# Kernel optimization log

Measured on AMD Instinct MI355X. Metric: run time of the kernel, lower is better.

## Reference

```python
import jax, jax.numpy as jnp
import numpy as np

C = 256
NUM_HEADS = 8
GROUPS = 32
EPS = 1e-5


def setup_inputs() -> dict:
    key = jax.random.key(0)
    ks = jax.random.split(key, 7)
    B, D, H, W = 1, 16, 16, 16
    x = jax.random.normal(ks[0], (B, C, D, H, W), dtype=jnp.float32)
    # GroupNorm affine params (torch default: weight=1, bias=0; randomize slightly)
    gn_gamma = 1.0 + 0.02 * jax.random.normal(ks[1], (C,), dtype=jnp.float32)
    gn_beta = 0.02 * jax.random.normal(ks[2], (C,), dtype=jnp.float32)
    # 1x1x1 Conv3d == pointwise linear over channels
    qkv_w = jax.random.normal(ks[3], (3 * C, C), dtype=jnp.float32) / np.sqrt(C)
    qkv_b = 0.01 * jax.random.normal(ks[4], (3 * C,), dtype=jnp.float32)
    proj_w = jax.random.normal(ks[5], (C, C), dtype=jnp.float32) / np.sqrt(C)
    proj_b = 0.01 * jax.random.normal(ks[6], (C,), dtype=jnp.float32)
    return {"x": x, "gn_gamma": gn_gamma, "gn_beta": gn_beta,
            "qkv_w": qkv_w, "qkv_b": qkv_b, "proj_w": proj_w, "proj_b": proj_b}


def _group_norm(x, gamma, beta):
    B, Cc, D, H, W = x.shape
    xg = x.reshape(B, GROUPS, -1)  # [B, G, (C/G)*D*H*W]
    mean = xg.mean(axis=2, keepdims=True)
    var = xg.var(axis=2, keepdims=True)
    xn = ((xg - mean) * jax.lax.rsqrt(var + EPS)).reshape(B, Cc, D, H, W)
    return xn * gamma[None, :, None, None, None] + beta[None, :, None, None, None]


def reference(x, gn_gamma, gn_beta, qkv_w, qkv_b, proj_w, proj_b):
    B, Cc, D, H, W = x.shape
    N = D * H * W
    heads = NUM_HEADS
    hd = Cc // heads
    scale = hd ** -0.5

    xn = _group_norm(x, gn_gamma, gn_beta)
    # 1x1x1 conv -> pointwise linear over channel dim
    h = jnp.einsum('bcn,oc->bon', xn.reshape(B, Cc, N), qkv_w) + qkv_b[None, :, None]
    # match torch: reshape(B,3,heads,hd,N).permute(1,0,2,4,3)
    qkv = h.reshape(B, 3, heads, hd, N).transpose(1, 0, 2, 4, 3)  # [3,B,heads,N,hd]
    q, k, v = qkv[0], qkv[1], qkv[2]
    attn = jax.nn.softmax(jnp.einsum('bhnd,bhmd->bhnm', q, k) * scale, axis=-1)
    out = jnp.einsum('bhnm,bhmd->bhnd', attn, v)  # [B,heads,N,hd]
    # match torch: transpose(1,2).reshape(B,C,D,H,W)
    out = out.transpose(0, 2, 1, 3).reshape(B, Cc, D, H, W)
    out = jnp.einsum('bcn,oc->bon', out.reshape(B, Cc, N), proj_w) + proj_b[None, :, None]
    return x + out.reshape(B, Cc, D, H, W)
```

## Files before the change

kernel.cpp:

```cpp
#include <hip/hip_runtime.h>
#include <hip/hip_bf16.h>
#include <cstddef>
#include <cstdint>

#define NTOK 4096
#define CCH  256
#define HEADS 8
#define HD    32
#define QSCALE 0.25503494f

typedef __attribute__((ext_vector_type(8)))  short short8;
typedef __attribute__((ext_vector_type(4)))  short short4v;
typedef __attribute__((ext_vector_type(16))) float f32x16;

__device__ __forceinline__ unsigned short f2bf(float x) {
    unsigned u = __builtin_bit_cast(unsigned, x);
    u = (u + 0x7fffu + ((u >> 16) & 1u)) >> 16;
    return (unsigned short)u;
}
__device__ __forceinline__ unsigned packbf2(float a, float b) {
    unsigned r;
    asm("v_cvt_pk_bf16_f32 %0, %1, %2" : "=v"(r) : "v"(a), "v"(b));
    return r;
}
__device__ __forceinline__ float exp2hw(float x) {
    float r;
    asm("v_exp_f32 %0, %1" : "=v"(r) : "v"(x));
    return r;
}

#define GLDS(gsrc, ldst) \
  __builtin_amdgcn_global_load_lds((const __attribute__((address_space(1))) unsigned int*)(const void*)(gsrc), \
                                   (__attribute__((address_space(3))) unsigned int*)(void*)(ldst), 16, 0, 0)

#define CROW(r, hi) (((r) & 3) + 8 * ((r) >> 2) + 4 * (hi))

__global__ __launch_bounds__(256) void gn_part_kernel(
    const float* __restrict__ X, float2* __restrict__ part)
{
    int c = blockIdx.x, tid = threadIdx.x;
    const float4* xr = (const float4*)(X + (size_t)c * NTOK);
    float s = 0.f, ss = 0.f;
    #pragma unroll
    for (int i = 0; i < 4; i++) {
        float4 v = xr[tid + i * 256];
        s  += (v.x + v.y) + (v.z + v.w);
        ss += (v.x*v.x + v.y*v.y) + (v.z*v.z + v.w*v.w);
    }
    #pragma unroll
    for (int off = 32; off >= 1; off >>= 1) {
        s  += __shfl_down(s, off, 64);
        ss += __shfl_down(ss, off, 64);
    }
    __shared__ float rs[4], rss[4];
    int wid = tid >> 6, lane = tid & 63;
    if (lane == 0) { rs[wid] = s; rss[wid] = ss; }
    __syncthreads();
    if (tid == 0) {
        part[c] = make_float2(rs[0] + rs[1] + rs[2] + rs[3],
                              rss[0] + rss[1] + rss[2] + rss[3]);
    }
}

__global__ __launch_bounds__(256) void prep_kernel(
    const float* __restrict__ X, const float2* __restrict__ part,
    const float* __restrict__ gamma, const float* __restrict__ beta,
    const float* __restrict__ qkvw, const float* __restrict__ projw,
    unsigned short* __restrict__ Xt, unsigned short* __restrict__ Wqb,
    unsigned short* __restrict__ Wpb)
{
    int bi = blockIdx.x, tid = threadIdx.x;
    if (bi >= 256) {
        const float* src; unsigned short* dst;
        if (bi < 268) { src = qkvw + (size_t)(bi - 256) * 16384; dst = Wqb + (size_t)(bi - 256) * 16384; }
        else          { src = projw + (size_t)(bi - 268) * 16384; dst = Wpb + (size_t)(bi - 268) * 16384; }
        #pragma unroll
        for (int i = 0; i < 16; i++) {
            float4 v = *(const float4*)(src + (size_t)tid * 4 + (size_t)i * 1024);
            short4v w;
            w[0] = (short)f2bf(v.x); w[1] = (short)f2bf(v.y);
            w[2] = (short)f2bf(v.z); w[3] = (short)f2bf(v.w);
            *(short4v*)(dst + (size_t)tid * 4 + (size_t)i * 1024) = w;
        }
        return;
    }
    __shared__ float plds[64 * 65];
    __shared__ float gmean[8], grstd[8];
    int ci = bi >> 6, ni = bi & 63;
    if (tid < 8) {
        int g = ci * 8 + tid;
        float s = 0.f, ss = 0.f;
        #pragma unroll
        for (int k = 0; k < 8; k++) {
            float2 p = part[g * 8 + k];
            s += p.x; ss += p.y;
        }
        float mean = s * (1.f / 32768.f);
        float var  = ss * (1.f / 32768.f) - mean * mean;
        gmean[tid] = mean;
        grstd[tid] = rsqrtf(var + 1e-5f);
    }
    __syncthreads();
    #pragma unroll
    for (int i = 0; i < 4; i++) {
        int cl = (tid >> 4) + i * 16;
        int c  = ci * 64 + cl;
        int gl = cl >> 3;
        float scv = gamma[c] * grstd[gl];
        float tcv = beta[c] - gmean[gl] * scv;
        float4 v = *(const float4*)(X + (size_t)c * NTOK + ni * 64 + (tid & 15) * 4);
        float* row = plds + cl * 65 + (tid & 15) * 4;
        row[0] = v.x * scv + tcv; row[1] = v.y * scv + tcv;
        row[2] = v.z * scv + tcv; row[3] = v.w * scv + tcv;
    }
    __syncthreads();
    int nw = tid >> 2, c4 = (tid & 3) * 16;
    unsigned short tmp[16];
    #pragma unroll
    for (int i = 0; i < 16; i++) tmp[i] = f2bf(plds[(c4 + i) * 65 + nw]);
    unsigned short* dst = Xt + (size_t)(ni * 64 + nw) * CCH + ci * 64 + c4;
    *(short8*)dst       = *(short8*)&tmp[0];
    *(short8*)(dst + 8) = *(short8*)&tmp[8];
}

__global__ __launch_bounds__(256) void qkv_mfma_kernel(
    const unsigned short* __restrict__ Wqb, const unsigned short* __restrict__ Xt,
    const float* __restrict__ qkvb,
    unsigned short* __restrict__ Qb, unsigned short* __restrict__ Kbf,
    unsigned short* __restrict__ Vtb)
{
    __shared__ __align__(16) char vlds[16384];
    const int tid = threadIdx.x;
    const int wid = tid >> 6, lane = tid & 63;
    const int l31 = lane & 31, hi = lane >> 5;
    const int bo = blockIdx.x >> 5, ng = blockIdx.x & 31;
    const int o0 = bo * 32;
    const int n0 = ng * 128 + wid * 32;

    const unsigned short* ap = Xt + (size_t)(n0 + l31) * CCH + hi * 8;
    const unsigned short* bp = Wqb + (size_t)(o0 + l31) * CCH + hi * 8;

    f32x16 acc;
    #pragma unroll
    for (int i = 0; i < 16; i++) acc[i] = 0.f;
    #pragma unroll 4
    for (int ks = 0; ks < 16; ks++) {
        short8 af = *(const short8*)(ap + ks * 16);
        short8 bf = *(const short8*)(bp + ks * 16);
        acc = __builtin_amdgcn_mfma_f32_32x32x16_bf16(af, bf, acc, 0, 0, 0);
    }

    const int t3 = bo >> 3;
    const int h  = (o0 >> 5) & 7;
    const float bias = qkvb[o0 + l31];

    if (t3 != 2) {
        unsigned short* dst = ((t3 == 0) ? Qb : Kbf) + (size_t)h * NTOK * HD + l31;
        const float scl = (t3 == 0) ? QSCALE : 1.0f;
        #pragma unroll
        for (int r = 0; r < 16; r++) {
            int n = n0 + CROW(r, hi);
            dst[(size_t)n * HD] = f2bf((acc[r] + bias) * scl);
        }
    } else {
        char* my = vlds + wid * 4096;
        #pragma unroll
        for (int r = 0; r < 16; r++) {
            int row = CROW(r, hi);
            *(float*)(my + row * 128 + ((l31 * 4) ^ ((row & 7) << 4))) = acc[r] + bias;
        }
        unsigned short tmp[16];
        #pragma unroll
        for (int i = 0; i < 16; i++) {
            int n = hi * 16 + i;
            tmp[i] = f2bf(*(const float*)(my + n * 128 + ((l31 * 4) ^ ((n & 7) << 4))));
        }
        unsigned short* vd = Vtb + ((size_t)h * HD + l31) * NTOK + n0 + hi * 16;
        *(short8*)vd       = *(short8*)&tmp[0];
        *(short8*)(vd + 8) = *(short8*)&tmp[8];
    }
}

__global__ __launch_bounds__(256, 2) void attn_mfma_kernel(
    const unsigned short* __restrict__ Qb, const unsigned short* __restrict__ Kbf,
    const unsigned short* __restrict__ Vtb, unsigned short* __restrict__ att_t)
{
    __shared__ __align__(16) char ldsbuf[65536];
    __shared__ float lsum[4][64];
    const int tid = threadIdx.x;
    const int wid = tid >> 6, lane = tid & 63;
    const int l31 = lane & 31, hi = lane >> 5;
    const int bid = blockIdx.x;
    const int h    = bid & 7;
    const int g    = bid >> 3;
    const int base = g & 15;
    const int j0   = (g >> 4) * 64;

    const char* Khb = (const char*)(Kbf + (size_t)h * NTOK * HD) + (size_t)wid * 65536;
    const char* Vhb = (const char*)(Vtb + (size_t)h * HD * NTOK) + (size_t)wid * 2048;

    const char* srcK0 = Khb + l31 * 64 + hi * 16;
    const char* srcK1 = Khb + l31 * 64 + 32 + hi * 16;
    const char* srcV0 = Vhb + (size_t)l31 * 8192 + hi * 16;
    const char* srcV1 = Vhb + (size_t)l31 * 8192 + 32 + hi * 16;
    char* myLDS = ldsbuf + wid * 16384;

#define STAGE(tt, bb) do { \
    char* _db = myLDS + (bb) * 4096; \
    GLDS(srcK0 + (size_t)(tt) * 2048, _db); \
    GLDS(srcK1 + (size_t)(tt) * 2048, _db + 1024); \
    GLDS(srcV0 + (size_t)(tt) * 64,   _db + 2048); \
    GLDS(srcV1 + (size_t)(tt) * 64,   _db + 3072); \
} while (0)

    const int koff0 = l31 * 16 + hi * 512;
    const int koff1 = l31 * 16 + 1024 + hi * 512;
    const int voff0 = 2048 + koff0;
    const int voff1 = 2048 + koff1;

    const unsigned short* qpA = Qb + ((size_t)h * NTOK + base + 16 * (size_t)(j0 + l31)) * HD + hi * 8;
    const unsigned short* qpB = qpA + (size_t)32 * 16 * HD;
    short8 qfA0 = *(const short8*)qpA;
    short8 qfA1 = *(const short8*)(qpA + 16);
    short8 qfB0 = *(const short8*)qpB;
    short8 qfB1 = *(const short8*)(qpB + 16);

    f32x16 oaccA, oaccB;
    #pragma unroll
    for (int i = 0; i < 16; i++) { oaccA[i] = 0.f; oaccB[i] = 0.f; }
    const f32x16 zero = oaccA;
    float lA = 0.f, lB = 0.f;

    STAGE(0, 0);
    STAGE(1, 1);
    STAGE(2, 2);

    #pragma unroll 1
    for (int t = 0; t < 32; t++) {
        asm volatile("s_waitcnt vmcnt(8)" ::: "memory");
        const int ts = (t + 3 < 32) ? (t + 3) : 31;
        STAGE(ts, (t + 3) & 3);

        const char* kb = myLDS + (t & 3) * 4096;
        short8 kf0 = *(const short8*)(kb + koff0);
        short8 kf1 = *(const short8*)(kb + koff1);

        f32x16 sA = __builtin_amdgcn_mfma_f32_32x32x16_bf16(kf0, qfA0, zero, 0, 0, 0);
        f32x16 sB = __builtin_amdgcn_mfma_f32_32x32x16_bf16(kf0, qfB0, zero, 0, 0, 0);
        sA = __builtin_amdgcn_mfma_f32_32x32x16_bf16(kf1, qfA1, sA, 0, 0, 0);
        sB = __builtin_amdgcn_mfma_f32_32x32x16_bf16(kf1, qfB1, sB, 0, 0, 0);

        short8 vf0 = *(const short8*)(kb + voff0);
        short8 vf1 = *(const short8*)(kb + voff1);

        float pA[16], pB[16];
        #pragma unroll
        for (int r = 0; r < 16; r++) pA[r] = exp2hw(sA[r]);
        #pragma unroll
        for (int r = 0; r < 16; r++) pB[r] = exp2hw(sB[r]);
        lA += (((pA[0]+pA[1]) + (pA[2]+pA[3])) + ((pA[4]+pA[5]) + (pA[6]+pA[7])))
            + (((pA[8]+pA[9]) + (pA[10]+pA[11])) + ((pA[12]+pA[13]) + (pA[14]+pA[15])));
        lB += (((pB[0]+pB[1]) + (pB[2]+pB[3])) + ((pB[4]+pB[5]) + (pB[6]+pB[7])))
            + (((pB[8]+pB[9]) + (pB[10]+pB[11])) + ((pB[12]+pB[13]) + (pB[14]+pB[15])));

        #pragma unroll
        for (int m = 0; m < 2; m++) {
            const int b8 = m * 8;
            unsigned A0 = packbf2(pA[b8 + 0], pA[b8 + 1]);
            unsigned A1 = packbf2(pA[b8 + 2], pA[b8 + 3]);
            unsigned B0 = packbf2(pA[b8 + 4], pA[b8 + 5]);
            unsigned B1 = packbf2(pA[b8 + 6], pA[b8 + 7]);
            asm volatile("v_permlane32_swap_b32 %0, %1" : "+v"(A0), "+v"(B0));
            asm volatile("v_permlane32_swap_b32 %0, %1" : "+v"(A1), "+v"(B1));
            union { unsigned u[4]; short8 v; } pa;
            pa.u[0] = A0; pa.u[1] = A1; pa.u[2] = B0; pa.u[3] = B1;
            oaccA = __builtin_amdgcn_mfma_f32_32x32x16_bf16(
                pa.v, (m == 0) ? vf0 : vf1, oaccA, 0, 0, 0);
        }
        #pragma unroll
        for (int m = 0; m < 2; m++) {
            const int b8 = m * 8;
            unsigned A0 = packbf2(pB[b8 + 0], pB[b8 + 1]);
            unsigned A1 = packbf2(pB[b8 + 2], pB[b8 + 3]);
            unsigned B0 = packbf2(pB[b8 + 4], pB[b8 + 5]);
            unsigned B1 = packbf2(pB[b8 + 6], pB[b8 + 7]);
            asm volatile("v_permlane32_swap_b32 %0, %1" : "+v"(A0), "+v"(B0));
            asm volatile("v_permlane32_swap_b32 %0, %1" : "+v"(A1), "+v"(B1));
            union { unsigned u[4]; short8 v; } pa;
            pa.u[0] = A0; pa.u[1] = A1; pa.u[2] = B0; pa.u[3] = B1;
            oaccB = __builtin_amdgcn_mfma_f32_32x32x16_bf16(
                pa.v, (m == 0) ? vf0 : vf1, oaccB, 0, 0, 0);
        }
    }
#undef STAGE

    lA += __shfl_xor(lA, 32, 64);
    lB += __shfl_xor(lB, 32, 64);
    char* st = myLDS;
    #pragma unroll
    for (int r = 0; r < 16; r++) {
        int rowA = CROW(r, hi);
        *(float*)(st + rowA * 148 + l31 * 4) = oaccA[r];
        *(float*)(st + (rowA + 32) * 148 + l31 * 4) = oaccB[r];
    }
    if (lane < 32) { lsum[wid][l31] = lA; lsum[wid][32 + l31] = lB; }
    __syncthreads();

    const int d = tid >> 3, q8 = (tid & 7) * 8;
    unsigned short ob[8];
    #pragma unroll
    for (int i = 0; i < 8; i++) {
        int q = q8 + i;
        float lt = (lsum[0][q] + lsum[1][q]) + (lsum[2][q] + lsum[3][q]);
        int so = q * 148 + d * 4;
        float a = (*(const float*)(ldsbuf + so)          + *(const float*)(ldsbuf + 16384 + so))
                + (*(const float*)(ldsbuf + 32768 + so)  + *(const float*)(ldsbuf + 49152 + so));
        ob[i] = f2bf(a / lt);
    }
    unsigned short* dst = att_t + (size_t)(base * 256 + h * 32 + d) * CCH + j0 + q8;
    *(short8*)dst = *(short8*)ob;
}

__global__ __launch_bounds__(256) void proj_mfma_kernel(
    const unsigned short* __restrict__ Wpb, const unsigned short* __restrict__ att_t,
    const float* __restrict__ X, const float* __restrict__ pb,
    float* __restrict__ out)
{
    const int tid = threadIdx.x;
    const int wid = tid >> 6, lane = tid & 63;
    const int l31 = lane & 31, hi = lane >> 5;
    const int ot = blockIdx.x >> 5, pg = blockIdx.x & 31;
    const int o0 = ot * 32;
    const int p0 = pg * 128 + wid * 32;

    const unsigned short* ap = Wpb + (size_t)(o0 + l31) * CCH + hi * 8;
    const unsigned short* bp = att_t + (size_t)(p0 + l31) * CCH + hi * 8;

    f32x16 acc;
    #pragma unroll
    for (int i = 0; i < 16; i++) acc[i] = 0.f;
    #pragma unroll 4
    for (int ks = 0; ks < 16; ks++) {
        short8 af = *(const short8*)(ap + ks * 16);
        short8 bf = *(const short8*)(bp + ks * 16);
        acc = __builtin_amdgcn_mfma_f32_32x32x16_bf16(af, bf, acc, 0, 0, 0);
    }
    #pragma unroll
    for (int r = 0; r < 16; r++) {
        int o = o0 + CROW(r, hi);
        size_t ofs = (size_t)o * NTOK + p0 + l31;
        out[ofs] = X[ofs] + pb[o] + acc[r];
    }
}

extern "C" void kernel_launch(void* const* d_in, const int* in_sizes, int n_in,
                              void* d_out, int out_size, void* d_ws, size_t ws_size,
                              hipStream_t stream)
{
    const float* x     = (const float*)d_in[0];
    const float* gamma = (const float*)d_in[1];
    const float* beta  = (const float*)d_in[2];
    const float* qkvw  = (const float*)d_in[3];
    const float* qkvb  = (const float*)d_in[4];
    const float* projw = (const float*)d_in[5];
    const float* projb = (const float*)d_in[6];
    float* out = (float*)d_out;

    char* ws = (char*)d_ws;
    const size_t MB = 1024 * 1024;
    float2* part = (float2*)ws;
    unsigned short* Xt    = (unsigned short*)(ws + 4096);
    unsigned short* Wqb   = (unsigned short*)(ws + 4096 + 2*MB);
    unsigned short* Wpb   = Wqb + 768 * 256;
    unsigned short* Qb    = Wpb + 256 * 256;
    unsigned short* Kbf   = Qb + HEADS * NTOK * HD;
    unsigned short* Vtb   = Kbf + HEADS * NTOK * HD;
    unsigned short* att_t = Vtb + HEADS * NTOK * HD;

    gn_part_kernel<<<256, 256, 0, stream>>>(x, part);
    prep_kernel<<<272, 256, 0, stream>>>(x, part, gamma, beta, qkvw, projw, Xt, Wqb, Wpb);
    qkv_mfma_kernel<<<768, 256, 0, stream>>>(Wqb, Xt, qkvb, Qb, Kbf, Vtb);
    attn_mfma_kernel<<<512, 256, 0, stream>>>(Qb, Kbf, Vtb, att_t);
    proj_mfma_kernel<<<256, 256, 0, stream>>>(Wpb, att_t, x, projb, out);
}
```

Baseline: 66.55 us.

## Load K/V fragments directly to registers instead of LDS-staged async copies

Replaces the 4-deep global_load_lds pipeline that staged K and V tiles through 64KB of shared memory with direct per-lane global loads into registers, double-buffered by manually unrolling the key loop by two. The LDS footprint shrinks to a small padded stash used only for the final cross-wave reduction, and the occupancy hint of 2 blocks per SM is dropped from launch bounds. The aim is to cut LDS traffic and the wait/stage overhead. The trade-off is a shallower prefetch distance, so global latency may be less hidden, plus higher register pressure.

```diff
diff --git a/kernel.cpp b/kernel.cpp
--- a/kernel.cpp
+++ b/kernel.cpp
@@ -28,10 +28,6 @@
     asm("v_exp_f32 %0, %1" : "=v"(r) : "v"(x));
     return r;
 }
-
-#define GLDS(gsrc, ldst) \
-  __builtin_amdgcn_global_load_lds((const __attribute__((address_space(1))) unsigned int*)(const void*)(gsrc), \
-                                   (__attribute__((address_space(3))) unsigned int*)(void*)(ldst), 16, 0, 0)
 
 #define CROW(r, hi) (((r) & 3) + 8 * ((r) >> 2) + 4 * (hi))
 
@@ -181,11 +177,11 @@
     }
 }
 
-__global__ __launch_bounds__(256, 2) void attn_mfma_kernel(
+__global__ __launch_bounds__(256) void attn_mfma_kernel(
     const unsigned short* __restrict__ Qb, const unsigned short* __restrict__ Kbf,
     const unsigned short* __restrict__ Vtb, unsigned short* __restrict__ att_t)
 {
-    __shared__ __align__(16) char ldsbuf[65536];
+    __shared__ float stash[4][64][37];
     __shared__ float lsum[4][64];
     const int tid = threadIdx.x;
     const int wid = tid >> 6, lane = tid & 63;
@@ -196,27 +192,8 @@
     const int base = g & 15;
     const int j0   = (g >> 4) * 64;
 
-    const char* Khb = (const char*)(Kbf + (size_t)h * NTOK * HD) + (size_t)wid * 65536;
-    const char* Vhb = (const char*)(Vtb + (size_t)h * HD * NTOK) + (size_t)wid * 2048;
-
-    const char* srcK0 = Khb + l31 * 64 + hi * 16;
-    const char* srcK1 = Khb + l31 * 64 + 32 + hi * 16;
-    const char* srcV0 = Vhb + (size_t)l31 * 8192 + hi * 16;
-    const char* srcV1 = Vhb + (size_t)l31 * 8192 + 32 + hi * 16;
-    char* myLDS = ldsbuf + wid * 16384;
-
-#define STAGE(tt, bb) do { \
-    char* _db = myLDS + (bb) * 4096; \
-    GLDS(srcK0 + (size_t)(tt) * 2048, _db); \
-    GLDS(srcK1 + (size_t)(tt) * 2048, _db + 1024); \
-    GLDS(srcV0 + (size_t)(tt) * 64,   _db + 2048); \
-    GLDS(srcV1 + (size_t)(tt) * 64,   _db + 3072); \
-} while (0)
-
-    const int koff0 = l31 * 16 + hi * 512;
-    const int koff1 = l31 * 16 + 1024 + hi * 512;
-    const int voff0 = 2048 + koff0;
-    const int voff1 = 2048 + koff1;
+    const unsigned short* kp = Kbf + ((size_t)h * NTOK + wid * 1024 + l31) * HD + hi * 8;
+    const unsigned short* vp = Vtb + ((size_t)h * HD + l31) * NTOK + wid * 1024 + hi * 8;
 
     const unsigned short* qpA = Qb + ((size_t)h * NTOK + base + 16 * (size_t)(j0 + l31)) * HD + hi * 8;
     const unsigned short* qpB = qpA + (size_t)32 * 16 * HD;
@@ -231,77 +208,77 @@
     const f32x16 zero = oaccA;
     float lA = 0.f, lB = 0.f;
 
-    STAGE(0, 0);
-    STAGE(1, 1);
-    STAGE(2, 2);
+#define ATTN_BODY(KF0, KF1, VF0, VF1) do {                                     \
+    f32x16 sA = __builtin_amdgcn_mfma_f32_32x32x16_bf16(KF0, qfA0, zero, 0, 0, 0); \
+    sA = __builtin_amdgcn_mfma_f32_32x32x16_bf16(KF1, qfA1, sA, 0, 0, 0);      \
+    f32x16 sB = __builtin_amdgcn_mfma_f32_32x32x16_bf16(KF0, qfB0, zero, 0, 0, 0); \
+    sB = __builtin_amdgcn_mfma_f32_32x32x16_bf16(KF1, qfB1, sB, 0, 0, 0);      \
+    float pA[16], pB[16];                                                      \
+    _Pragma("unroll") for (int r = 0; r < 16; r++) pA[r] = exp2hw(sA[r]);      \
+    _Pragma("unroll") for (int r = 0; r < 16; r++) pB[r] = exp2hw(sB[r]);      \
+    lA += (((pA[0]+pA[1]) + (pA[2]+pA[3])) + ((pA[4]+pA[5]) + (pA[6]+pA[7])))  \
+        + (((pA[8]+pA[9]) + (pA[10]+pA[11])) + ((pA[12]+pA[13]) + (pA[14]+pA[15]))); \
+    lB += (((pB[0]+pB[1]) + (pB[2]+pB[3])) + ((pB[4]+pB[5]) + (pB[6]+pB[7])))  \
+        + (((pB[8]+pB[9]) + (pB[10]+pB[11])) + ((pB[12]+pB[13]) + (pB[14]+pB[15]))); \
+    _Pragma("unroll")                                                          \
+    for (int m = 0; m < 2; m++) {                                              \
+        const int b8 = m * 8;                                                  \
+        unsigned A0 = packbf2(pA[b8 + 0], pA[b8 + 1]);                         \
+        unsigned A1 = packbf2(pA[b8 + 2], pA[b8 + 3]);                         \
+        unsigned B0 = packbf2(pA[b8 + 4], pA[b8 + 5]);                         \
+        unsigned B1 = packbf2(pA[b8 + 6], pA[b8 + 7]);                         \
+        asm volatile("v_permlane32_swap_b32 %0, %1" : "+v"(A0), "+v"(B0));     \
+        asm volatile("v_permlane32_swap_b32 %0, %1" : "+v"(A1), "+v"(B1));     \
+        union { unsigned u[4]; short8 v; } pa;                                 \
+        pa.u[0] = A0; pa.u[1] = A1; pa.u[2] = B0; pa.u[3] = B1;                \
+        oaccA = __builtin_amdgcn_mfma_f32_32x32x16_bf16(                       \
+            pa.v, (m == 0) ? (VF0) : (VF1), oaccA, 0, 0, 0);                   \
+    }                                                                          \
+    _Pragma("unroll")                                                          \
+    for (int m = 0; m < 2; m++) {                                              \
+        const int b8 = m * 8;                                                  \
+        unsigned A0 = packbf2(pB[b8 + 0], pB[b8 + 1]);                         \
+        unsigned A1 = packbf2(pB[b8 + 2], pB[b8 + 3]);                         \
+        unsigned B0 = packbf2(pB[b8 + 4], pB[b8 + 5]);                         \
+        unsigned B1 = packbf2(pB[b8 + 6], pB[b8 + 7]);                         \
+        asm volatile("v_permlane32_swap_b32 %0, %1" : "+v"(A0), "+v"(B0));     \
+        asm volatile("v_permlane32_swap_b32 %0, %1" : "+v"(A1), "+v"(B1));     \
+        union { unsigned u[4]; short8 v; } pa;                                 \
+        pa.u[0] = A0; pa.u[1] = A1; pa.u[2] = B0; pa.u[3] = B1;                \
+        oaccB = __builtin_amdgcn_mfma_f32_32x32x16_bf16(                       \
+            pa.v, (m == 0) ? (VF0) : (VF1), oaccB, 0, 0, 0);                   \
+    }                                                                          \
+} while (0)
+
+    short8 kf0a = *(const short8*)(kp);
+    short8 kf1a = *(const short8*)(kp + 16);
+    short8 vf0a = *(const short8*)(vp);
+    short8 vf1a = *(const short8*)(vp + 16);
 
     #pragma unroll 1
-    for (int t = 0; t < 32; t++) {
-        asm volatile("s_waitcnt vmcnt(8)" ::: "memory");
-        const int ts = (t + 3 < 32) ? (t + 3) : 31;
-        STAGE(ts, (t + 3) & 3);
-
-        const char* kb = myLDS + (t & 3) * 4096;
-        short8 kf0 = *(const short8*)(kb + koff0);
-        short8 kf1 = *(const short8*)(kb + koff1);
-
-        f32x16 sA = __builtin_amdgcn_mfma_f32_32x32x16_bf16(kf0, qfA0, zero, 0, 0, 0);
-        f32x16 sB = __builtin_amdgcn_mfma_f32_32x32x16_bf16(kf0, qfB0, zero, 0, 0, 0);
-        sA = __builtin_amdgcn_mfma_f32_32x32x16_bf16(kf1, qfA1, sA, 0, 0, 0);
-        sB = __builtin_amdgcn_mfma_f32_32x32x16_bf16(kf1, qfB1, sB, 0, 0, 0);
-
-        short8 vf0 = *(const short8*)(kb + voff0);
-        short8 vf1 = *(const short8*)(kb + voff1);
-
-        float pA[16], pB[16];
-        #pragma unroll
-        for (int r = 0; r < 16; r++) pA[r] = exp2hw(sA[r]);
-        #pragma unroll
-        for (int r = 0; r < 16; r++) pB[r] = exp2hw(sB[r]);
-        lA += (((pA[0]+pA[1]) + (pA[2]+pA[3])) + ((pA[4]+pA[5]) + (pA[6]+pA[7])))
-            + (((pA[8]+pA[9]) + (pA[10]+pA[11])) + ((pA[12]+pA[13]) + (pA[14]+pA[15])));
-        lB += (((pB[0]+pB[1]) + (pB[2]+pB[3])) + ((pB[4]+pB[5]) + (pB[6]+pB[7])))
-            + (((pB[8]+pB[9]) + (pB[10]+pB[11])) + ((pB[12]+pB[13]) + (pB[14]+pB[15])));
-
-        #pragma unroll
-        for (int m = 0; m < 2; m++) {
-            const int b8 = m * 8;
-            unsigned A0 = packbf2(pA[b8 + 0], pA[b8 + 1]);
-            unsigned A1 = packbf2(pA[b8 + 2], pA[b8 + 3]);
-            unsigned B0 = packbf2(pA[b8 + 4], pA[b8 + 5]);
-            unsigned B1 = packbf2(pA[b8 + 6], pA[b8 + 7]);
-            asm volatile("v_permlane32_swap_b32 %0, %1" : "+v"(A0), "+v"(B0));
-            asm volatile("v_permlane32_swap_b32 %0, %1" : "+v"(A1), "+v"(B1));
-            union { unsigned u[4]; short8 v; } pa;
-            pa.u[0] = A0; pa.u[1] = A1; pa.u[2] = B0; pa.u[3] = B1;
-            oaccA = __builtin_amdgcn_mfma_f32_32x32x16_bf16(
-                pa.v, (m == 0) ? vf0 : vf1, oaccA, 0, 0, 0);
-        }
-        #pragma unroll
-        for (int m = 0; m < 2; m++) {
-            const int b8 = m * 8;
-            unsigned A0 = packbf2(pB[b8 + 0], pB[b8 + 1]);
-            unsigned A1 = packbf2(pB[b8 + 2], pB[b8 + 3]);
-            unsigned B0 = packbf2(pB[b8 + 4], pB[b8 + 5]);
-            unsigned B1 = packbf2(pB[b8 + 6], pB[b8 + 7]);
-            asm volatile("v_permlane32_swap_b32 %0, %1" : "+v"(A0), "+v"(B0));
-            asm volatile("v_permlane32_swap_b32 %0, %1" : "+v"(A1), "+v"(B1));
-            union { unsigned u[4]; short8 v; } pa;
-            pa.u[0] = A0; pa.u[1] = A1; pa.u[2] = B0; pa.u[3] = B1;
-            oaccB = __builtin_amdgcn_mfma_f32_32x32x16_bf16(
-                pa.v, (m == 0) ? vf0 : vf1, oaccB, 0, 0, 0);
-        }
-    }
-#undef STAGE
+    for (int t = 0; t < 32; t += 2) {
+        const int t1 = t + 1;
+        short8 kf0b = *(const short8*)(kp + t1 * 1024);
+        short8 kf1b = *(const short8*)(kp + t1 * 1024 + 16);
+        short8 vf0b = *(const short8*)(vp + t1 * 32);
+        short8 vf1b = *(const short8*)(vp + t1 * 32 + 16);
+        ATTN_BODY(kf0a, kf1a, vf0a, vf1a);
+        const int t2 = (t + 2 < 32) ? (t + 2) : 31;
+        kf0a = *(const short8*)(kp + t2 * 1024);
+        kf1a = *(const short8*)(kp + t2 * 1024 + 16);
+        vf0a = *(const short8*)(vp + t2 * 32);
+        vf1a = *(const short8*)(vp + t2 * 32 + 16);
+        ATTN_BODY(kf0b, kf1b, vf0b, vf1b);
+    }
+#undef ATTN_BODY
 
     lA += __shfl_xor(lA, 32, 64);
     lB += __shfl_xor(lB, 32, 64);
-    char* st = myLDS;
     #pragma unroll
     for (int r = 0; r < 16; r++) {
         int rowA = CROW(r, hi);
-        *(float*)(st + rowA * 148 + l31 * 4) = oaccA[r];
-        *(float*)(st + (rowA + 32) * 148 + l31 * 4) = oaccB[r];
+        stash[wid][rowA][l31] = oaccA[r];
+        stash[wid][rowA + 32][l31] = oaccB[r];
     }
     if (lane < 32) { lsum[wid][l31] = lA; lsum[wid][32 + l31] = lB; }
     __syncthreads();
@@ -312,9 +289,7 @@
     for (int i = 0; i < 8; i++) {
         int q = q8 + i;
         float lt = (lsum[0][q] + lsum[1][q]) + (lsum[2][q] + lsum[3][q]);
-        int so = q * 148 + d * 4;
-        float a = (*(const float*)(ldsbuf + so)          + *(const float*)(ldsbuf + 16384 + so))
-                + (*(const float*)(ldsbuf + 32768 + so)  + *(const float*)(ldsbuf + 49152 + so));
+        float a = (stash[0][q][d] + stash[1][q][d]) + (stash[2][q][d] + stash[3][q][d]);
         ob[i] = f2bf(a / lt);
     }
     unsigned short* dst = att_t + (size_t)(base * 256 + h * 32 + d) * CCH + j0 + q8;
```

Measured after the change: 62.59 us. -6.0%, faster.
